# Kernel tuning notes

Measured on AMD Instinct MI355X. Metric: run time of the kernel, lower is better.

The kernel has to match this reference:

```python
import jax, jax.numpy as jnp
import numpy as np

DIM = 1024
HEADS = 16
DIM_HEAD = 64
INNER = HEADS * DIM_HEAD  # 1024


def setup_inputs() -> dict:
    key = jax.random.key(0)
    kx, kqkv, kwo, kbo = jax.random.split(key, 4)
    x = jax.random.normal(kx, (4, 2048, DIM), dtype=jnp.float32)
    # nn.Linear weights stored as [out, in]; we keep [in, out] for x @ W
    w_qkv = jax.random.normal(kqkv, (DIM, 3 * INNER), dtype=jnp.float32) * (1.0 / np.sqrt(DIM))
    w_out = jax.random.normal(kwo, (INNER, DIM), dtype=jnp.float32) * (1.0 / np.sqrt(INNER))
    b_out = jax.random.normal(kbo, (DIM,), dtype=jnp.float32) * 0.01
    return {"x": x, "w_qkv": w_qkv, "w_out": w_out, "b_out": b_out}


def reference(x, w_qkv, w_out, b_out):
    b, n, _ = x.shape
    scale = 1.0 / np.sqrt(DIM_HEAD)
    qkv = x @ w_qkv  # [b, n, 3*inner]
    q, k, v = jnp.split(qkv, 3, axis=-1)
    # [b, n, inner] -> [b, h, n, d]
    reshape = lambda z: z.reshape(b, n, HEADS, DIM_HEAD).transpose(0, 2, 1, 3)
    q, k, v = reshape(q), reshape(k), reshape(v)
    sim = jnp.einsum('bhid,bhjd->bhij', q, k) * scale
    attn = jax.nn.softmax(sim, axis=-1)  # dropout p=0.0 -> identity
    out = jnp.einsum('bhij,bhjd->bhid', attn, v)
    out = out.transpose(0, 2, 1, 3).reshape(b, n, INNER)
    return out @ w_out + b_out
```

## Files before the change

kernel.cpp:

```cpp
#include <hip/hip_runtime.h>
#include <hip/hip_fp16.h>

typedef __attribute__((ext_vector_type(4))) float f32x4;
typedef __attribute__((ext_vector_type(8))) _Float16 h8;
typedef __attribute__((ext_vector_type(4))) _Float16 h4;

__device__ __forceinline__ void gld16(const _Float16* g, _Float16* l) {
  __builtin_amdgcn_global_load_lds(
      (const __attribute__((address_space(1))) void*)g,
      (__attribute__((address_space(3))) void*)l, 16, 0, 0);
}

__global__ void cvt_f32_h(const float* __restrict__ in, _Float16* __restrict__ out, int n8) {
  for (int i = blockIdx.x * blockDim.x + threadIdx.x; i < n8; i += gridDim.x * blockDim.x) {
    const f32x4* p = (const f32x4*)(in + (size_t)i * 8);
    f32x4 a = p[0], b = p[1];
    h8 o;
    o[0] = (_Float16)a[0]; o[1] = (_Float16)a[1]; o[2] = (_Float16)a[2]; o[3] = (_Float16)a[3];
    o[4] = (_Float16)b[0]; o[5] = (_Float16)b[1]; o[6] = (_Float16)b[2]; o[7] = (_Float16)b[3];
    *(h8*)(out + (size_t)i * 8) = o;
  }
}

__global__ void transpose_cvt(const float* __restrict__ in, _Float16* __restrict__ out, int R, int C) {
  __shared__ float tile[32][33];
  const int tx = threadIdx.x & 31, ty = threadIdx.x >> 5;
  const int c = blockIdx.x * 32 + tx;
#pragma unroll
  for (int j = 0; j < 32; j += 8) {
    int r = blockIdx.y * 32 + ty + j;
    tile[ty + j][tx] = in[(size_t)r * C + c];
  }
  __syncthreads();
#pragma unroll
  for (int j = 0; j < 32; j += 8) {
    out[(size_t)(blockIdx.x * 32 + ty + j) * R + blockIdx.y * 32 + tx] = (_Float16)tile[tx][ty + j];
  }
}

template <int EPI>
__global__ __launch_bounds__(256, 2)
void gemm_kernel(const _Float16* __restrict__ A, const _Float16* __restrict__ Bt,
                 float* __restrict__ outF, const float* __restrict__ bias,
                 _Float16* __restrict__ q_h, _Float16* __restrict__ k_h,
                 _Float16* __restrict__ v_t, const int Nn, const int K) {
  __shared__ _Float16 As[128 * 64];
  __shared__ _Float16 Bs[128 * 64];
  const int tid = threadIdx.x;
  const int wid = tid >> 6, lane = tid & 63;
  const int g = lane >> 4, r16 = lane & 15;
  const int wr = wid >> 1, wc = wid & 1;
  const int row0 = blockIdx.x * 128;
  const int col0 = blockIdx.y * 128;
  f32x4 acc[4][4] = {};
  const int sr = tid >> 3, sc = tid & 7;
  const _Float16* ag = A + (size_t)(row0 + sr) * K + sc * 8;
  const _Float16* bg = Bt + (size_t)(col0 + sr) * K + sc * 8;

  for (int kt = 0; kt < K; kt += 64) {
    __syncthreads();
#pragma unroll
    for (int i = 0; i < 4; ++i)
      gld16(ag + (size_t)i * 32 * K + kt, As + i * 2048 + wid * 512);
#pragma unroll
    for (int i = 0; i < 4; ++i)
      gld16(bg + (size_t)i * 32 * K + kt, Bs + i * 2048 + wid * 512);
    __syncthreads();

#pragma unroll
    for (int kk = 0; kk < 2; ++kk) {
      h8 af[4], bf[4];
#pragma unroll
      for (int mt = 0; mt < 4; ++mt)
        af[mt] = *(const h8*)(As + (wr * 64 + mt * 16 + r16) * 64 + kk * 32 + g * 8);
#pragma unroll
      for (int nt = 0; nt < 4; ++nt)
        bf[nt] = *(const h8*)(Bs + (wc * 64 + nt * 16 + r16) * 64 + kk * 32 + g * 8);
#pragma unroll
      for (int mt = 0; mt < 4; ++mt)
#pragma unroll
        for (int nt = 0; nt < 4; ++nt)
          acc[mt][nt] = __builtin_amdgcn_mfma_f32_16x16x32_f16(af[mt], bf[nt], acc[mt][nt], 0, 0, 0);
    }
  }

  if (EPI == 0) {
    const float qscale = 0.125f * 1.44269504088896340736f;
#pragma unroll
    for (int mt = 0; mt < 4; ++mt) {
#pragma unroll
      for (int nt = 0; nt < 4; ++nt) {
        const int j = col0 + wc * 64 + nt * 16 + r16;
        const int which = j >> 10;
        const int hd = j & 1023;
        const int hh = hd >> 6, dd = hd & 63;
#pragma unroll
        for (int rg = 0; rg < 4; ++rg) {
          const int mm = row0 + wr * 64 + mt * 16 + g * 4 + rg;
          const int b = mm >> 11, n = mm & 2047;
          const size_t bh = (size_t)(b * 16 + hh);
          const float v = acc[mt][nt][rg];
          if (which == 0)      q_h[(bh * 2048 + n) * 64 + dd] = (_Float16)(v * qscale);
          else if (which == 1) k_h[(bh * 2048 + n) * 64 + dd] = (_Float16)v;
          else                 v_t[(bh * 64 + dd) * 2048 + n] = (_Float16)v;
        }
      }
    }
  } else {
#pragma unroll
    for (int mt = 0; mt < 4; ++mt) {
#pragma unroll
      for (int nt = 0; nt < 4; ++nt) {
        const int j = col0 + wc * 64 + nt * 16 + r16;
        const float bv = bias[j];
#pragma unroll
        for (int rg = 0; rg < 4; ++rg) {
          const int mm = row0 + wr * 64 + mt * 16 + g * 4 + rg;
          outF[(size_t)mm * Nn + j] = acc[mt][nt][rg] + bv;
        }
      }
    }
  }
}

__device__ __forceinline__ void stage_kv(const _Float16* Kg, const _Float16* Vg,
                                         _Float16* KsB, _Float16* VsB,
                                         int kv0, int sr, int sc8, int wid) {
#pragma unroll
  for (int i = 0; i < 2; ++i) {
    int r = i * 32 + sr;
    gld16(Kg + (size_t)(kv0 + r) * 64 + (sc8 ^ ((r & 7) * 8)), KsB + i * 2048 + wid * 512);
    gld16(Vg + (size_t)r * 2048 + kv0 + (sc8 ^ ((r & 7) * 8)), VsB + i * 2048 + wid * 512);
  }
}

__global__ __launch_bounds__(256, 2)
void attn_kernel(const _Float16* __restrict__ Qall, const _Float16* __restrict__ Kall,
                 const _Float16* __restrict__ Vtall, _Float16* __restrict__ Oall) {
  __shared__ _Float16 Qs[256 * 64];
  __shared__ _Float16 Ks[2][64 * 64];
  __shared__ _Float16 Vs[2][64 * 64];
  const int tid = threadIdx.x;
  const int wid = tid >> 6, lane = tid & 63;
  const int g = lane >> 4, r16 = lane & 15;
  const int blk = (blockIdx.x & 7) * 64 + (blockIdx.x >> 3);
  const int qt = blk & 7;
  const int bh = blk >> 3;
  const _Float16* Qg = Qall + (size_t)bh * (2048 * 64);
  const _Float16* Kg = Kall + (size_t)bh * (2048 * 64);
  const _Float16* Vg = Vtall + (size_t)bh * (2048 * 64);
  const int q0 = qt * 256;
  const int sr = tid >> 3, sc8 = (tid & 7) * 8;

#pragma unroll
  for (int i = 0; i < 8; ++i) {
    int r = i * 32 + sr;
    gld16(Qg + (size_t)(q0 + r) * 64 + (sc8 ^ ((r & 7) * 8)), Qs + i * 2048 + wid * 512);
  }
  stage_kv(Kg, Vg, Ks[0], Vs[0], 0, sr, sc8, wid);
  __syncthreads();

  h8 qf[4][2];
#pragma unroll
  for (int qb = 0; qb < 4; ++qb) {
    const int qrow = wid * 64 + qb * 16 + r16;
#pragma unroll
    for (int kd = 0; kd < 2; ++kd)
      qf[qb][kd] = *(const h8*)(Qs + qrow * 64 + ((kd * 32 + g * 8) ^ ((qrow & 7) * 8)));
  }

  f32x4 ot[4][4] = {};
  float m[4], l[4];
#pragma unroll
  for (int qb = 0; qb < 4; ++qb) { m[qb] = -3.0e38f; l[qb] = 0.f; }

  auto compute = [&](const _Float16* KsB, const _Float16* VsB) {
    h8 kf[4][2];
#pragma unroll
    for (int kb = 0; kb < 4; ++kb) {
      const int krow = kb * 16 + r16;
#pragma unroll
      for (int kd = 0; kd < 2; ++kd)
        kf[kb][kd] = *(const h8*)(KsB + krow * 64 + ((kd * 32 + g * 8) ^ ((krow & 7) * 8)));
    }
    h4 vf[4][4];
#pragma unroll
    for (int db = 0; db < 4; ++db) {
      const int vrow = db * 16 + r16;
#pragma unroll
      for (int kg = 0; kg < 4; ++kg)
        vf[db][kg] = *(const h4*)(VsB + vrow * 64 + ((kg * 16 + g * 4) ^ ((vrow & 7) * 8)));
    }
#pragma unroll
    for (int qb = 0; qb < 4; ++qb) {
      f32x4 st[4];
#pragma unroll
      for (int kb = 0; kb < 4; ++kb) {
        f32x4 s = {};
        s = __builtin_amdgcn_mfma_f32_16x16x32_f16(kf[kb][0], qf[qb][0], s, 0, 0, 0);
        s = __builtin_amdgcn_mfma_f32_16x16x32_f16(kf[kb][1], qf[qb][1], s, 0, 0, 0);
        st[kb] = s;
      }
      float pmax = st[0][0];
#pragma unroll
      for (int kb = 0; kb < 4; ++kb)
#pragma unroll
        for (int rg = 0; rg < 4; ++rg) pmax = fmaxf(pmax, st[kb][rg]);
      pmax = fmaxf(pmax, __shfl_xor(pmax, 16));
      pmax = fmaxf(pmax, __shfl_xor(pmax, 32));
      if (__any(pmax > m[qb] + 8.f)) {
        const float mn = fmaxf(m[qb], pmax);
        const float corr = __builtin_amdgcn_exp2f(m[qb] - mn);
        l[qb] *= corr;
#pragma unroll
        for (int db = 0; db < 4; ++db) ot[qb][db] *= corr;
        m[qb] = mn;
      }
      float rs = 0.f;
      h4 pb[4];
#pragma unroll
      for (int kb = 0; kb < 4; ++kb)
#pragma unroll
        for (int rg = 0; rg < 4; ++rg) {
          float p = __builtin_amdgcn_exp2f(st[kb][rg] - m[qb]);
          rs += p;
          pb[kb][rg] = (_Float16)p;
        }
      rs += __shfl_xor(rs, 16);
      rs += __shfl_xor(rs, 32);
      l[qb] += rs;
#pragma unroll
      for (int db = 0; db < 4; ++db)
#pragma unroll
        for (int kg = 0; kg < 4; ++kg)
          ot[qb][db] = __builtin_amdgcn_mfma_f32_16x16x16f16(vf[db][kg], pb[kg], ot[qb][db], 0, 0, 0);
    }
  };

#pragma unroll 1
  for (int tt = 0; tt < 16; ++tt) {
    stage_kv(Kg, Vg, Ks[1], Vs[1], (tt * 2 + 1) * 64, sr, sc8, wid);
    compute(Ks[0], Vs[0]);
    __syncthreads();
    if (tt < 15) stage_kv(Kg, Vg, Ks[0], Vs[0], (tt * 2 + 2) * 64, sr, sc8, wid);
    compute(Ks[1], Vs[1]);
    __syncthreads();
  }

#pragma unroll
  for (int qb = 0; qb < 4; ++qb) {
    const float inv = 1.f / l[qb];
    const int qrow = wid * 64 + qb * 16 + r16;
    const int x = (qrow & 7) * 8;
#pragma unroll
    for (int db = 0; db < 4; ++db) {
      h4 o;
#pragma unroll
      for (int rg = 0; rg < 4; ++rg) o[rg] = (_Float16)(ot[qb][db][rg] * inv);
      *(h4*)(Qs + qrow * 64 + ((db * 16 + g * 4) ^ x)) = o;
    }
  }
  __syncthreads();
  const int bb = bh >> 4, hh = bh & 15;
#pragma unroll
  for (int i = 0; i < 8; ++i) {
    const int idx = tid + i * 256;
    const int q = idx >> 3, c = idx & 7;
    h8 vv = *(const h8*)(Qs + q * 64 + ((c * 8) ^ ((q & 7) * 8)));
    *(h8*)(Oall + ((size_t)(bb * 2048 + q0 + q) * 1024 + hh * 64 + c * 8)) = vv;
  }
}

extern "C" void kernel_launch(void* const* d_in, const int* in_sizes, int n_in,
                              void* d_out, int out_size, void* d_ws, size_t ws_size,
                              hipStream_t stream) {
  const float* x     = (const float*)d_in[0];
  const float* w_qkv = (const float*)d_in[1];
  const float* w_out = (const float*)d_in[2];
  const float* b_out = (const float*)d_in[3];
  float* out = (float*)d_out;

  char* ws = (char*)d_ws;
  _Float16* x_h    = (_Float16*)(ws);
  _Float16* wqkv_t = (_Float16*)(ws + 16777216);
  _Float16* wout_t = (_Float16*)(ws + 23068672);
  _Float16* q_h    = (_Float16*)(ws + 25165824);
  _Float16* k_h    = (_Float16*)(ws + 41943040);
  _Float16* v_t    = (_Float16*)(ws + 58720256);
  _Float16* o_h    = (_Float16*)(ws + 75497472);

  hipLaunchKernelGGL(cvt_f32_h, dim3(2048), dim3(256), 0, stream, x, x_h, (8192 * 1024) / 8);
  hipLaunchKernelGGL(transpose_cvt, dim3(96, 32), dim3(256), 0, stream, w_qkv, wqkv_t, 1024, 3072);
  hipLaunchKernelGGL(transpose_cvt, dim3(32, 32), dim3(256), 0, stream, w_out, wout_t, 1024, 1024);

  hipLaunchKernelGGL((gemm_kernel<0>), dim3(64, 24), dim3(256), 0, stream,
                     x_h, wqkv_t, nullptr, nullptr, q_h, k_h, v_t, 3072, 1024);

  hipLaunchKernelGGL(attn_kernel, dim3(512), dim3(256), 0, stream, q_h, k_h, v_t, o_h);

  hipLaunchKernelGGL((gemm_kernel<1>), dim3(64, 8), dim3(256), 0, stream,
                     o_h, wout_t, out, b_out, nullptr, nullptr, nullptr, 1024, 1024);
}
```

Before: 224.1 us.

## Compute softmax row sums via MFMA with ones vector and pack probabilities

Replaces the per-lane scalar accumulation and cross-lane shuffle reduction of the softmax denominator with an extra MFMA that multiplies a ones vector by the fp16 probabilities, accumulating the row sum in matrix-core registers. It also packs probabilities to fp16 with the round-toward-zero packed convert, reorders the QK MFMAs so the four independent chains interleave, and uses a tree max reduction. This removes VALU adds and shuffles but adds four MFMAs per block and sums the rounded fp16 probabilities, which changes numerics slightly and adds accumulator registers.

```diff
diff --git a/kernel.cpp b/kernel.cpp
--- a/kernel.cpp
+++ b/kernel.cpp
@@ -4,11 +4,21 @@
 typedef __attribute__((ext_vector_type(4))) float f32x4;
 typedef __attribute__((ext_vector_type(8))) _Float16 h8;
 typedef __attribute__((ext_vector_type(4))) _Float16 h4;
+typedef __attribute__((ext_vector_type(2))) _Float16 h2;
+typedef __attribute__((ext_vector_type(2))) __fp16 fp16x2;
 
 __device__ __forceinline__ void gld16(const _Float16* g, _Float16* l) {
   __builtin_amdgcn_global_load_lds(
       (const __attribute__((address_space(1))) void*)g,
       (__attribute__((address_space(3))) void*)l, 16, 0, 0);
+}
+
+__device__ __forceinline__ h4 pack4(float p0, float p1, float p2, float p3) {
+  fp16x2 lo = __builtin_amdgcn_cvt_pkrtz(p0, p1);
+  fp16x2 hi = __builtin_amdgcn_cvt_pkrtz(p2, p3);
+  h2 lo2 = __builtin_bit_cast(h2, lo);
+  h2 hi2 = __builtin_bit_cast(h2, hi);
+  return __builtin_shufflevector(lo2, hi2, 0, 1, 2, 3);
 }
 
 __global__ void cvt_f32_h(const float* __restrict__ in, _Float16* __restrict__ out, int n8) {
@@ -170,9 +180,11 @@
   }
 
   f32x4 ot[4][4] = {};
-  float m[4], l[4];
-#pragma unroll
-  for (int qb = 0; qb < 4; ++qb) { m[qb] = -3.0e38f; l[qb] = 0.f; }
+  f32x4 lacc[4] = {};
+  float m[4];
+#pragma unroll
+  for (int qb = 0; qb < 4; ++qb) m[qb] = -3.0e38f;
+  const h4 ones = {(_Float16)1.f, (_Float16)1.f, (_Float16)1.f, (_Float16)1.f};
 
   auto compute = [&](const _Float16* KsB, const _Float16* VsB) {
     h8 kf[4][2];
@@ -196,44 +208,44 @@
       f32x4 st[4];
 #pragma unroll
       for (int kb = 0; kb < 4; ++kb) {
-        f32x4 s = {};
-        s = __builtin_amdgcn_mfma_f32_16x16x32_f16(kf[kb][0], qf[qb][0], s, 0, 0, 0);
-        s = __builtin_amdgcn_mfma_f32_16x16x32_f16(kf[kb][1], qf[qb][1], s, 0, 0, 0);
-        st[kb] = s;
-      }
-      float pmax = st[0][0];
+        f32x4 z = {};
+        st[kb] = __builtin_amdgcn_mfma_f32_16x16x32_f16(kf[kb][0], qf[qb][0], z, 0, 0, 0);
+      }
 #pragma unroll
       for (int kb = 0; kb < 4; ++kb)
-#pragma unroll
-        for (int rg = 0; rg < 4; ++rg) pmax = fmaxf(pmax, st[kb][rg]);
+        st[kb] = __builtin_amdgcn_mfma_f32_16x16x32_f16(kf[kb][1], qf[qb][1], st[kb], 0, 0, 0);
+
+      float a0 = fmaxf(fmaxf(st[0][0], st[0][1]), fmaxf(st[0][2], st[0][3]));
+      float a1 = fmaxf(fmaxf(st[1][0], st[1][1]), fmaxf(st[1][2], st[1][3]));
+      float a2 = fmaxf(fmaxf(st[2][0], st[2][1]), fmaxf(st[2][2], st[2][3]));
+      float a3 = fmaxf(fmaxf(st[3][0], st[3][1]), fmaxf(st[3][2], st[3][3]));
+      float pmax = fmaxf(fmaxf(a0, a1), fmaxf(a2, a3));
       pmax = fmaxf(pmax, __shfl_xor(pmax, 16));
       pmax = fmaxf(pmax, __shfl_xor(pmax, 32));
       if (__any(pmax > m[qb] + 8.f)) {
         const float mn = fmaxf(m[qb], pmax);
         const float corr = __builtin_amdgcn_exp2f(m[qb] - mn);
-        l[qb] *= corr;
+        lacc[qb] *= corr;
 #pragma unroll
         for (int db = 0; db < 4; ++db) ot[qb][db] *= corr;
         m[qb] = mn;
       }
-      float rs = 0.f;
       h4 pb[4];
 #pragma unroll
-      for (int kb = 0; kb < 4; ++kb)
-#pragma unroll
-        for (int rg = 0; rg < 4; ++rg) {
-          float p = __builtin_amdgcn_exp2f(st[kb][rg] - m[qb]);
-          rs += p;
-          pb[kb][rg] = (_Float16)p;
-        }
-      rs += __shfl_xor(rs, 16);
-      rs += __shfl_xor(rs, 32);
-      l[qb] += rs;
-#pragma unroll
-      for (int db = 0; db < 4; ++db)
-#pragma unroll
-        for (int kg = 0; kg < 4; ++kg)
+      for (int kb = 0; kb < 4; ++kb) {
+        float p0 = __builtin_amdgcn_exp2f(st[kb][0] - m[qb]);
+        float p1 = __builtin_amdgcn_exp2f(st[kb][1] - m[qb]);
+        float p2 = __builtin_amdgcn_exp2f(st[kb][2] - m[qb]);
+        float p3 = __builtin_amdgcn_exp2f(st[kb][3] - m[qb]);
+        pb[kb] = pack4(p0, p1, p2, p3);
+      }
+#pragma unroll
+      for (int kg = 0; kg < 4; ++kg) {
+#pragma unroll
+        for (int db = 0; db < 4; ++db)
           ot[qb][db] = __builtin_amdgcn_mfma_f32_16x16x16f16(vf[db][kg], pb[kg], ot[qb][db], 0, 0, 0);
+        lacc[qb] = __builtin_amdgcn_mfma_f32_16x16x16f16(ones, pb[kg], lacc[qb], 0, 0, 0);
+      }
     }
   };
 
@@ -249,7 +261,7 @@
 
 #pragma unroll
   for (int qb = 0; qb < 4; ++qb) {
-    const float inv = 1.f / l[qb];
+    const float inv = 1.f / lacc[qb][0];
     const int qrow = wid * 64 + qb * 16 + r16;
     const int x = (qrow & 7) * 8;
 #pragma unroll
```

Measured after the change: 230.3 us. 1.03x slower.
